# Optimization experiments

Hardware: AMD Instinct MI355X
Metric: run time of the kernel (lower is better)

The kernel has to match this reference:

```python
import jax, jax.numpy as jnp
import numpy as np

NUM_FEATURES = 10000
EMBED_DIM = 64
BATCH = 16384


def setup_inputs() -> dict:
    key = jax.random.key(0)
    k1, k2 = jax.random.split(key)
    # binary multi-hot indicator matrix [B, F]
    multi_hot = jax.random.randint(k1, (BATCH, NUM_FEATURES), 0, 2, dtype=jnp.int32)
    # xavier_uniform init: bound = sqrt(6 / (fan_in + fan_out))
    bound = float(np.sqrt(6.0 / (NUM_FEATURES + EMBED_DIM)))
    embed_matrix = jax.random.uniform(
        k2, (NUM_FEATURES, EMBED_DIM), minval=-bound, maxval=bound, dtype=jnp.float32
    )
    return {"multi_hot": multi_hot, "embed_matrix": embed_matrix}


def reference(multi_hot, embed_matrix):
    # multi_hot.float() @ embed_matrix  -> [B, D]
    return jnp.matmul(multi_hot.astype(embed_matrix.dtype), embed_matrix)
```

## Files before the change

kernel.cpp:

```cpp
#include <hip/hip_runtime.h>


typedef int    int4v   __attribute__((ext_vector_type(4)));
typedef float  float4v __attribute__((ext_vector_type(4)));
typedef float  f32x4   __attribute__((ext_vector_type(4)));
typedef short  bf16x8  __attribute__((ext_vector_type(8)));
typedef unsigned int uint4v __attribute__((ext_vector_type(4)));

constexpr int M_DIM  = 16384;
constexpr int K_DIM  = 10000;
constexpr int N_DIM  = 64;
constexpr int WORDS  = 160;
constexpr int SLOTS  = 10240;
constexpr int SPLIT  = 4;
constexpr int CH_SEG = WORDS / SPLIT;

__device__ __forceinline__ unsigned f2bf(float x) {
    unsigned u = __builtin_bit_cast(unsigned, x);
    u += 0x7FFFu + ((u >> 16) & 1u);
    return u >> 16;
}

__device__ __forceinline__ int orig_of(int s) {
    const int grp = s >> 8, rem = s & 255, j = rem >> 6, l = rem & 63;
    return (grp << 8) + 4 * l + j;
}

__global__ __launch_bounds__(256) void pack(const int* __restrict__ mh,
                                            const float* __restrict__ em,
                                            unsigned long long* __restrict__ pa,
                                            unsigned short* __restrict__ bt,
                                            float* __restrict__ out) {
    const int b = blockIdx.x, tid = threadIdx.x;
    if (b < 4096) {
        const int lane = tid & 63, wv = tid >> 6;
        const int row  = b * 4 + wv;
        const int4v* rp = (const int4v*)(mh + (long long)row * K_DIM);
        unsigned long long* wp = pa + (long long)row * WORDS;

        auto emit = [&](int g, int4v v) {
            unsigned long long w0 = __ballot(v[0] != 0);
            unsigned long long w1 = __ballot(v[1] != 0);
            unsigned long long w2 = __ballot(v[2] != 0);
            unsigned long long w3 = __ballot(v[3] != 0);
            if (lane < 4) {
                unsigned long long w = lane == 0 ? w0 : lane == 1 ? w1
                                     : lane == 2 ? w2 : w3;
                wp[g * 4 + lane] = w;
            }
        };

        int4v vc = __builtin_nontemporal_load(rp + lane);
        for (int g = 0; g < 38; ++g) {
            int4v vn = __builtin_nontemporal_load(rp + (g + 1) * 64 + lane);
            emit(g, vc);
            vc = vn;
        }
        int4v vt = {};
        if (lane < 4) vt = rp[39 * 64 + lane];
        emit(38, vc);
        emit(39, vt);
    } else if (b < 4096 + 160) {
        const int s0 = (b - 4096) * 64;
        const int n = tid >> 2, q = tid & 3;
        unsigned u[8];
        #pragma unroll
        for (int i = 0; i < 8; ++i) {
            const int sA = s0 + q * 16 + 2 * i, sB = sA + 1;
            const int oA = orig_of(sA), oB = orig_of(sB);
            const unsigned lo = (oA < K_DIM) ? f2bf(em[oA * N_DIM + n]) : 0u;
            const unsigned hi = (oB < K_DIM) ? f2bf(em[oB * N_DIM + n]) : 0u;
            u[i] = lo | (hi << 16);
        }
        uint4v* dst = (uint4v*)(bt + (long long)n * SLOTS + s0 + q * 16);
        uint4v w0 = {u[0], u[1], u[2], u[3]};
        uint4v w1 = {u[4], u[5], u[6], u[7]};
        dst[0] = w0; dst[1] = w1;
    } else {
        const int b3 = b - 4256;
        float4v z = {0.f, 0.f, 0.f, 0.f};
        float4v* p = (float4v*)out;
        const int base = b3 * 256 + tid;
        #pragma unroll
        for (int i = 0; i < 4; ++i) p[base + i * 65536] = z;
    }
}

struct BF { bf16x8 f[4][2]; };

__global__ __launch_bounds__(256, 3) void mhe_gemm(
        const unsigned long long* __restrict__ pa,
        const unsigned short* __restrict__ bt,
        float* __restrict__ out) {
    const int tid  = threadIdx.x;
    const int lane = tid & 63;
    const int wv   = tid >> 6;
    const int w    = (int)blockIdx.x * 4 + wv;
    const int seg  = w >> 10;
    const int rw   = w & 1023;
    const int row0 = rw * 16;
    const int g    = lane >> 4;

    const unsigned long long* __restrict__ ap =
        pa + (long long)(row0 + (lane & 15)) * WORDS;

    const unsigned short* __restrict__ bpn[4];
    #pragma unroll
    for (int nt = 0; nt < 4; ++nt)
        bpn[nt] = bt + (long long)(nt * 16 + (lane & 15)) * SLOTS + g * 8;

    f32x4 acc[4] = {};

    auto expand = [&](unsigned byte) -> bf16x8 {
        uint4v x;
        #pragma unroll
        for (int i = 0; i < 4; ++i) {
            const unsigned t = byte >> (2 * i);
            x[i] = ((t & 1u) | ((t & 2u) << 15)) * 0x3F80u;
        }
        return __builtin_bit_cast(bf16x8, x);
    };

    auto loadB = [&](BF& bb, int c) {
        const int f0 = c * 64;
        #pragma unroll
        for (int nt = 0; nt < 4; ++nt) {
            bb.f[nt][0] = *(const bf16x8*)(bpn[nt] + f0);
            bb.f[nt][1] = *(const bf16x8*)(bpn[nt] + f0 + 32);
        }
    };

    auto computeChunk = [&](unsigned long long pw, const BF& bb) {
        const unsigned lo = (unsigned)pw, hi = (unsigned)(pw >> 32);
        bf16x8 a0 = expand((lo >> (8 * g)) & 255u);
        bf16x8 a1 = expand((hi >> (8 * g)) & 255u);
        #pragma unroll
        for (int nt = 0; nt < 4; ++nt) {
            acc[nt] = __builtin_amdgcn_mfma_f32_16x16x32_bf16(a0, bb.f[nt][0], acc[nt], 0, 0, 0);
            acc[nt] = __builtin_amdgcn_mfma_f32_16x16x32_bf16(a1, bb.f[nt][1], acc[nt], 0, 0, 0);
        }
    };

    const int c0 = seg * CH_SEG;
    unsigned long long pwA = ap[c0];
    BF bA; loadB(bA, c0);
    for (int c = c0; c < c0 + CH_SEG - 1; ++c) {
        unsigned long long pwB = ap[c + 1];
        BF bB; loadB(bB, c + 1);
        computeChunk(pwA, bA);
        pwA = pwB; bA = bB;
    }
    computeChunk(pwA, bA);

    const int crow = row0 + (g << 2);
    const int ccol = lane & 15;
    #pragma unroll
    for (int nt = 0; nt < 4; ++nt)
        #pragma unroll
        for (int i = 0; i < 4; ++i)
            unsafeAtomicAdd(&out[(long long)(crow + i) * N_DIM + nt * 16 + ccol],
                            acc[nt][i]);
}

extern "C" void kernel_launch(void* const* d_in, const int* in_sizes, int n_in,
                              void* d_out, int out_size, void* d_ws, size_t ws_size,
                              hipStream_t stream) {
    const int*   mh  = (const int*)d_in[0];
    const float* em  = (const float*)d_in[1];
    float*       out = (float*)d_out;
    unsigned long long* pa = (unsigned long long*)d_ws;
    unsigned short*     bt = (unsigned short*)((char*)d_ws +
                             (size_t)M_DIM * WORDS * 8);
    (void)in_sizes; (void)n_in; (void)out_size; (void)ws_size;

    pack<<<dim3(4512), dim3(256), 0, stream>>>(mh, em, pa, bt, out);
    mhe_gemm<<<dim3(1024), dim3(256), 0, stream>>>(pa, bt, out);
}
```

Measured before the change: 289.2 us.

## Fuse bit-packing into GEMM via shared memory and drop split-K atomics

Each block now packs the multi-hot rows for a 16-row tile straight into an LDS buffer and then runs the MFMA loop over the full K range, with each wave owning one 16-column slice of N. This removes the global round trip of the packed bitmask, the output zeroing pass and the split-K atomic adds, since outputs are written with plain stores. In exchange, the packing phase and the compute phase within a block no longer overlap, there are fewer blocks in flight, and every wave walks the whole K loop serially.

```diff
diff --git a/kernel.cpp b/kernel.cpp
--- a/kernel.cpp
+++ b/kernel.cpp
@@ -2,18 +2,17 @@
 
 
 typedef int    int4v   __attribute__((ext_vector_type(4)));
-typedef float  float4v __attribute__((ext_vector_type(4)));
 typedef float  f32x4   __attribute__((ext_vector_type(4)));
 typedef short  bf16x8  __attribute__((ext_vector_type(8)));
 typedef unsigned int uint4v __attribute__((ext_vector_type(4)));
 
-constexpr int M_DIM  = 16384;
-constexpr int K_DIM  = 10000;
-constexpr int N_DIM  = 64;
-constexpr int WORDS  = 160;
-constexpr int SLOTS  = 10240;
-constexpr int SPLIT  = 4;
-constexpr int CH_SEG = WORDS / SPLIT;
+constexpr int M_DIM = 16384;
+constexpr int K_DIM = 10000;
+constexpr int N_DIM = 64;
+constexpr int WORDS = 160;
+constexpr int WPAD  = 161;
+constexpr int SLOTS = 10240;
+constexpr int GPR   = 40;
 
 __device__ __forceinline__ unsigned f2bf(float x) {
     unsigned u = __builtin_bit_cast(unsigned, x);
@@ -26,90 +25,63 @@
     return (grp << 8) + 4 * l + j;
 }
 
-__global__ __launch_bounds__(256) void pack(const int* __restrict__ mh,
-                                            const float* __restrict__ em,
-                                            unsigned long long* __restrict__ pa,
-                                            unsigned short* __restrict__ bt,
-                                            float* __restrict__ out) {
-    const int b = blockIdx.x, tid = threadIdx.x;
-    if (b < 4096) {
-        const int lane = tid & 63, wv = tid >> 6;
-        const int row  = b * 4 + wv;
-        const int4v* rp = (const int4v*)(mh + (long long)row * K_DIM);
-        unsigned long long* wp = pa + (long long)row * WORDS;
-
-        auto emit = [&](int g, int4v v) {
-            unsigned long long w0 = __ballot(v[0] != 0);
-            unsigned long long w1 = __ballot(v[1] != 0);
-            unsigned long long w2 = __ballot(v[2] != 0);
-            unsigned long long w3 = __ballot(v[3] != 0);
-            if (lane < 4) {
-                unsigned long long w = lane == 0 ? w0 : lane == 1 ? w1
-                                     : lane == 2 ? w2 : w3;
-                wp[g * 4 + lane] = w;
-            }
-        };
-
-        int4v vc = __builtin_nontemporal_load(rp + lane);
-        for (int g = 0; g < 38; ++g) {
-            int4v vn = __builtin_nontemporal_load(rp + (g + 1) * 64 + lane);
-            emit(g, vc);
-            vc = vn;
-        }
-        int4v vt = {};
-        if (lane < 4) vt = rp[39 * 64 + lane];
-        emit(38, vc);
-        emit(39, vt);
-    } else if (b < 4096 + 160) {
-        const int s0 = (b - 4096) * 64;
-        const int n = tid >> 2, q = tid & 3;
-        unsigned u[8];
-        #pragma unroll
-        for (int i = 0; i < 8; ++i) {
-            const int sA = s0 + q * 16 + 2 * i, sB = sA + 1;
-            const int oA = orig_of(sA), oB = orig_of(sB);
-            const unsigned lo = (oA < K_DIM) ? f2bf(em[oA * N_DIM + n]) : 0u;
-            const unsigned hi = (oB < K_DIM) ? f2bf(em[oB * N_DIM + n]) : 0u;
-            u[i] = lo | (hi << 16);
-        }
-        uint4v* dst = (uint4v*)(bt + (long long)n * SLOTS + s0 + q * 16);
-        uint4v w0 = {u[0], u[1], u[2], u[3]};
-        uint4v w1 = {u[4], u[5], u[6], u[7]};
-        dst[0] = w0; dst[1] = w1;
-    } else {
-        const int b3 = b - 4256;
-        float4v z = {0.f, 0.f, 0.f, 0.f};
-        float4v* p = (float4v*)out;
-        const int base = b3 * 256 + tid;
-        #pragma unroll
-        for (int i = 0; i < 4; ++i) p[base + i * 65536] = z;
+__global__ __launch_bounds__(256) void btprep(const float* __restrict__ em,
+                                              unsigned short* __restrict__ bt) {
+    const int tid = threadIdx.x;
+    const int s0  = blockIdx.x * 64;
+    const int n = tid >> 2, q = tid & 3;
+    unsigned u[8];
+    #pragma unroll
+    for (int i = 0; i < 8; ++i) {
+        const int sA = s0 + q * 16 + 2 * i, sB = sA + 1;
+        const int oA = orig_of(sA), oB = orig_of(sB);
+        const unsigned lo = (oA < K_DIM) ? f2bf(em[oA * N_DIM + n]) : 0u;
+        const unsigned hi = (oB < K_DIM) ? f2bf(em[oB * N_DIM + n]) : 0u;
+        u[i] = lo | (hi << 16);
     }
+    uint4v* dst = (uint4v*)(bt + (long long)n * SLOTS + s0 + q * 16);
+    uint4v w0 = {u[0], u[1], u[2], u[3]};
+    uint4v w1 = {u[4], u[5], u[6], u[7]};
+    dst[0] = w0; dst[1] = w1;
 }
 
-struct BF { bf16x8 f[4][2]; };
+__global__ __launch_bounds__(256, 4) void fused(const int* __restrict__ mh,
+                                                const unsigned short* __restrict__ bt,
+                                                float* __restrict__ out) {
+    __shared__ unsigned long long pk[16][WPAD];
 
-__global__ __launch_bounds__(256, 3) void mhe_gemm(
-        const unsigned long long* __restrict__ pa,
-        const unsigned short* __restrict__ bt,
-        float* __restrict__ out) {
     const int tid  = threadIdx.x;
     const int lane = tid & 63;
     const int wv   = tid >> 6;
-    const int w    = (int)blockIdx.x * 4 + wv;
-    const int seg  = w >> 10;
-    const int rw   = w & 1023;
-    const int row0 = rw * 16;
-    const int g    = lane >> 4;
+    const long long r0 = (long long)blockIdx.x * 16;
 
-    const unsigned long long* __restrict__ ap =
-        pa + (long long)(row0 + (lane & 15)) * WORDS;
+    for (int r = 0; r < 16; ++r) {
+        const int* __restrict__ rp = mh + (r0 + r) * (long long)K_DIM;
+        #pragma unroll
+        for (int gg = 0; gg < 10; ++gg) {
+            const int g = wv + gg * 4;
+            int4v v = {};
+            if (g < GPR - 1 || lane < 4)
+                v = *(const int4v*)(rp + g * 256 + lane * 4);
+            unsigned long long b0 = __ballot(v[0] != 0);
+            unsigned long long b1 = __ballot(v[1] != 0);
+            unsigned long long b2 = __ballot(v[2] != 0);
+            unsigned long long b3 = __ballot(v[3] != 0);
+            if (lane < 4) {
+                unsigned long long w = lane == 0 ? b0 : lane == 1 ? b1
+                                     : lane == 2 ? b2 : b3;
+                pk[r][g * 4 + lane] = w;
+            }
+        }
+    }
+    __syncthreads();
 
-    const unsigned short* __restrict__ bpn[4];
-    #pragma unroll
-    for (int nt = 0; nt < 4; ++nt)
-        bpn[nt] = bt + (long long)(nt * 16 + (lane & 15)) * SLOTS + g * 8;
+    const int g = lane >> 4;
+    const unsigned short* __restrict__ bp =
+        bt + (long long)(wv * 16 + (lane & 15)) * SLOTS + g * 8;
+    const int ar = lane & 15;
 
-    f32x4 acc[4] = {};
+    f32x4 acc = {0.f, 0.f, 0.f, 0.f};
 
     auto expand = [&](unsigned byte) -> bf16x8 {
         uint4v x;
@@ -121,45 +93,33 @@
         return __builtin_bit_cast(bf16x8, x);
     };
 
-    auto loadB = [&](BF& bb, int c) {
-        const int f0 = c * 64;
-        #pragma unroll
-        for (int nt = 0; nt < 4; ++nt) {
-            bb.f[nt][0] = *(const bf16x8*)(bpn[nt] + f0);
-            bb.f[nt][1] = *(const bf16x8*)(bpn[nt] + f0 + 32);
-        }
-    };
-
-    auto computeChunk = [&](unsigned long long pw, const BF& bb) {
-        const unsigned lo = (unsigned)pw, hi = (unsigned)(pw >> 32);
+    unsigned long long awC = pk[ar][0];
+    bf16x8 b0C = *(const bf16x8*)(bp);
+    bf16x8 b1C = *(const bf16x8*)(bp + 32);
+    for (int c = 0; c < WORDS - 1; ++c) {
+        unsigned long long awN = pk[ar][c + 1];
+        bf16x8 b0N = *(const bf16x8*)(bp + (c + 1) * 64);
+        bf16x8 b1N = *(const bf16x8*)(bp + (c + 1) * 64 + 32);
+        const unsigned lo = (unsigned)awC, hi = (unsigned)(awC >> 32);
         bf16x8 a0 = expand((lo >> (8 * g)) & 255u);
         bf16x8 a1 = expand((hi >> (8 * g)) & 255u);
-        #pragma unroll
-        for (int nt = 0; nt < 4; ++nt) {
-            acc[nt] = __builtin_amdgcn_mfma_f32_16x16x32_bf16(a0, bb.f[nt][0], acc[nt], 0, 0, 0);
-            acc[nt] = __builtin_amdgcn_mfma_f32_16x16x32_bf16(a1, bb.f[nt][1], acc[nt], 0, 0, 0);
-        }
-    };
+        acc = __builtin_amdgcn_mfma_f32_16x16x32_bf16(a0, b0C, acc, 0, 0, 0);
+        acc = __builtin_amdgcn_mfma_f32_16x16x32_bf16(a1, b1C, acc, 0, 0, 0);
+        awC = awN; b0C = b0N; b1C = b1N;
+    }
+    {
+        const unsigned lo = (unsigned)awC, hi = (unsigned)(awC >> 32);
+        bf16x8 a0 = expand((lo >> (8 * g)) & 255u);
+        bf16x8 a1 = expand((hi >> (8 * g)) & 255u);
+        acc = __builtin_amdgcn_mfma_f32_16x16x32_bf16(a0, b0C, acc, 0, 0, 0);
+        acc = __builtin_amdgcn_mfma_f32_16x16x32_bf16(a1, b1C, acc, 0, 0, 0);
+    }
 
-    const int c0 = seg * CH_SEG;
-    unsigned long long pwA = ap[c0];
-    BF bA; loadB(bA, c0);
-    for (int c = c0; c < c0 + CH_SEG - 1; ++c) {
-        unsigned long long pwB = ap[c + 1];
-        BF bB; loadB(bB, c + 1);
-        computeChunk(pwA, bA);
-        pwA = pwB; bA = bB;
-    }
-    computeChunk(pwA, bA);
-
-    const int crow = row0 + (g << 2);
-    const int ccol = lane & 15;
+    const long long orow = r0 + g * 4;
+    const int ocol = wv * 16 + (lane & 15);
     #pragma unroll
-    for (int nt = 0; nt < 4; ++nt)
-        #pragma unroll
-        for (int i = 0; i < 4; ++i)
-            unsafeAtomicAdd(&out[(long long)(crow + i) * N_DIM + nt * 16 + ccol],
-                            acc[nt][i]);
+    for (int i = 0; i < 4; ++i)
+        out[(orow + i) * N_DIM + ocol] = acc[i];
 }
 
 extern "C" void kernel_launch(void* const* d_in, const int* in_sizes, int n_in,
@@ -168,11 +128,9 @@
     const int*   mh  = (const int*)d_in[0];
     const float* em  = (const float*)d_in[1];
     float*       out = (float*)d_out;
-    unsigned long long* pa = (unsigned long long*)d_ws;
-    unsigned short*     bt = (unsigned short*)((char*)d_ws +
-                             (size_t)M_DIM * WORDS * 8);
+    unsigned short* bt = (unsigned short*)d_ws;
     (void)in_sizes; (void)n_in; (void)out_size; (void)ws_size;
 
-    pack<<<dim3(4512), dim3(256), 0, stream>>>(mh, em, pa, bt, out);
-    mhe_gemm<<<dim3(1024), dim3(256), 0, stream>>>(pa, bt, out);
+    btprep<<<dim3(SLOTS / 64), dim3(256), 0, stream>>>(em, bt);
+    fused<<<dim3(M_DIM / 16), dim3(256), 0, stream>>>(mh, bt, out);
 }
```

Measured after the change: 275.5 us. 1.05x faster.
